# Performance work log

Measured on AMD Instinct MI355X. Metric: run time of the kernel, lower is better.

Reference implementation:

```python
import jax, jax.numpy as jnp
import numpy as np

EPS = 1e-5
NPOINT, K = 4096, 128
MLP = (64, 64, 128)
IN_CH = 3  # xyz only (Infea=0 -> use_feature=False)


def _conv_bn_relu(x, W, b, gamma, beta, mean, var):
    # 1x1 Conv2d == per-point channel GEMM: x [B,C,N,K], W [O,C]
    y = jnp.einsum('oc,bcnk->bonk', W, x) + b[None, :, None, None]
    inv = gamma / jnp.sqrt(var + EPS)
    y = y * inv[None, :, None, None] + (beta - mean * inv)[None, :, None, None]
    return jax.nn.relu(y)


def setup_inputs() -> dict:
    key = jax.random.key(0)
    ks = jax.random.split(key, 8)
    inp = {
        'grouped_pc': jax.random.normal(ks[0], (1, IN_CH, NPOINT, K), dtype=jnp.float32),
        'valid': (jax.random.uniform(ks[1], (1, 1, NPOINT, K)) > 0.3).astype(jnp.float32),
    }
    c_prev = IN_CH
    for i, c_out in enumerate(MLP, start=1):
        kw = jax.random.fold_in(ks[2], i)
        fan_in = c_prev  # kaiming_normal for 1x1 conv
        inp[f'W{i}'] = jax.random.normal(kw, (c_out, c_prev), dtype=jnp.float32) * np.sqrt(2.0 / fan_in)
        inp[f'b{i}'] = jnp.zeros((c_out,), dtype=jnp.float32)
        inp[f'gamma{i}'] = jnp.ones((c_out,), dtype=jnp.float32)
        inp[f'beta{i}'] = jnp.zeros((c_out,), dtype=jnp.float32)
        inp[f'mean{i}'] = jax.random.normal(jax.random.fold_in(ks[3], i), (c_out,), dtype=jnp.float32) * 0.1
        inp[f'var{i}'] = jax.random.uniform(jax.random.fold_in(ks[4], i), (c_out,), minval=0.5, maxval=1.5).astype(jnp.float32)
        c_prev = c_out
    return inp


def reference(grouped_pc, valid,
              W1, b1, gamma1, beta1, mean1, var1,
              W2, b2, gamma2, beta2, mean2, var2,
              W3, b3, gamma3, beta3, mean3, var3):
    x = _conv_bn_relu(grouped_pc, W1, b1, gamma1, beta1, mean1, var1)
    x = _conv_bn_relu(x, W2, b2, gamma2, beta2, mean2, var2)
    x = _conv_bn_relu(x, W3, b3, gamma3, beta3, mean3, var3)
    return x * valid  # validity mask broadcast over channels
```

## Files before the change

### kernel.cpp

```cpp
#include <hip/hip_runtime.h>
#include <math.h>

#define EPS 1e-5f
#define NPK (4096 * 128)

typedef __attribute__((ext_vector_type(8))) short bf16x8;
typedef __attribute__((ext_vector_type(4))) float f32x4;

__device__ __forceinline__ short f2bf(float f) {
    union { float f; unsigned u; } x; x.f = f;
    unsigned r = x.u + 0x7fffu + ((x.u >> 16) & 1u);
    return (short)(r >> 16);
}

#define WS_A1 0
#define WS_C1 192
#define WS_C2 256
#define WS_C3 320
#define WS_BF 448

__global__ void prep_kernel(
    const float* __restrict__ W1, const float* __restrict__ b1,
    const float* __restrict__ g1, const float* __restrict__ be1,
    const float* __restrict__ m1, const float* __restrict__ v1,
    const float* __restrict__ W2, const float* __restrict__ b2,
    const float* __restrict__ g2, const float* __restrict__ be2,
    const float* __restrict__ m2, const float* __restrict__ v2,
    const float* __restrict__ W3, const float* __restrict__ b3,
    const float* __restrict__ g3, const float* __restrict__ be3,
    const float* __restrict__ m3, const float* __restrict__ v3,
    float* __restrict__ ws)
{
    const int t = blockIdx.x * 256 + threadIdx.x;
    const int stride = gridDim.x * 256;
    if (t < 64) {
        float inv1 = g1[t] * rsqrtf(v1[t] + EPS);
        ws[WS_C1 + t] = b1[t] * inv1 + be1[t] - m1[t] * inv1;
        ws[WS_A1 + t * 3 + 0] = W1[t * 3 + 0] * inv1;
        ws[WS_A1 + t * 3 + 1] = W1[t * 3 + 1] * inv1;
        ws[WS_A1 + t * 3 + 2] = W1[t * 3 + 2] * inv1;
        float inv2 = g2[t] * rsqrtf(v2[t] + EPS);
        ws[WS_C2 + t] = b2[t] * inv2 + be2[t] - m2[t] * inv2;
    }
    if (t >= 128 && t < 256) {
        int o = t - 128;
        float inv3 = g3[o] * rsqrtf(v3[o] + EPS);
        ws[WS_C3 + o] = b3[o] * inv3 + be3[o] - m3[o] * inv3;
    }
    short* W2f = (short*)(ws + WS_BF);
    short* W3f = W2f + 64 * 64;
    for (int idx = t; idx < 64 * 64; idx += stride) {
        int j = idx & 7, lane = (idx >> 3) & 63, tile = idx >> 9;
        int nt = tile >> 1, ks = tile & 1;
        int o = nt * 16 + (lane & 15);
        int i = ks * 32 + (lane >> 4) * 8 + j;
        float inv = g2[o] * rsqrtf(v2[o] + EPS);
        W2f[idx] = f2bf(W2[o * 64 + i] * inv);
    }
    for (int idx = t; idx < 128 * 64; idx += stride) {
        int j = idx & 7, lane = (idx >> 3) & 63, tile = idx >> 9;
        int nt = tile >> 1, ks = tile & 1;
        int o = nt * 16 + (lane & 15);
        int i = ks * 32 + (lane >> 4) * 8 + j;
        float inv = g3[o] * rsqrtf(v3[o] + EPS);
        W3f[idx] = f2bf(W3[o * 64 + i] * inv);
    }
}

__global__ __launch_bounds__(256) void pointnet_mfma(
    const float* __restrict__ x, const float* __restrict__ valid,
    const float* __restrict__ ws, float* __restrict__ out)
{
    __shared__ short h1[128 * 72];
    __shared__ short h2[128 * 72];
    __shared__ float vld[128];

    const int t = threadIdx.x;
    const int pbase = blockIdx.x * 128;

    const float* __restrict__ A1 = ws + WS_A1;
    const float* __restrict__ C1 = ws + WS_C1;
    const float* __restrict__ C2 = ws + WS_C2;
    const float* __restrict__ C3 = ws + WS_C3;
    const short* __restrict__ W2f = (const short*)(ws + WS_BF);
    const short* __restrict__ W3f = W2f + 64 * 64;

    {
        const int pl = t & 127;
        const int half = t >> 7;
        const int pg = pbase + pl;
        const float x0 = x[pg];
        const float x1 = x[pg + NPK];
        const float x2 = x[pg + 2 * NPK];
        if (half == 0) vld[pl] = valid[pg];
        const int cb = half * 32;
#pragma unroll
        for (int g = 0; g < 4; ++g) {
            bf16x8 vb;
#pragma unroll
            for (int j = 0; j < 8; ++j) {
                const int ch = cb + g * 8 + j;
                float a = C1[ch];
                a = fmaf(A1[ch * 3 + 0], x0, a);
                a = fmaf(A1[ch * 3 + 1], x1, a);
                a = fmaf(A1[ch * 3 + 2], x2, a);
                vb[j] = f2bf(fmaxf(a, 0.0f));
            }
            *(bf16x8*)&h1[pl * 72 + cb + g * 8] = vb;
        }
    }
    __syncthreads();

    const int lane = t & 63;
    const int w = t >> 6;
    const int lanelo = lane & 15;
    const int quad = lane >> 4;

    {
        bf16x8 a[2][2];
#pragma unroll
        for (int mt = 0; mt < 2; ++mt)
#pragma unroll
            for (int ks = 0; ks < 2; ++ks)
                a[mt][ks] = *(const bf16x8*)&h1[(w * 32 + mt * 16 + lanelo) * 72 + ks * 32 + quad * 8];
#pragma unroll
        for (int nt = 0; nt < 4; ++nt) {
            bf16x8 b0 = *(const bf16x8*)&W2f[((nt * 2 + 0) * 64 + lane) * 8];
            bf16x8 b1 = *(const bf16x8*)&W2f[((nt * 2 + 1) * 64 + lane) * 8];
            const float bias = C2[nt * 16 + lanelo];
#pragma unroll
            for (int mt = 0; mt < 2; ++mt) {
                f32x4 acc = {0.f, 0.f, 0.f, 0.f};
                acc = __builtin_amdgcn_mfma_f32_16x16x32_bf16(a[mt][0], b0, acc, 0, 0, 0);
                acc = __builtin_amdgcn_mfma_f32_16x16x32_bf16(a[mt][1], b1, acc, 0, 0, 0);
#pragma unroll
                for (int r = 0; r < 4; ++r)
                    h2[(w * 32 + mt * 16 + quad * 4 + r) * 72 + nt * 16 + lanelo] =
                        f2bf(fmaxf(acc[r] + bias, 0.0f));
            }
        }
    }
    __syncthreads();

    {
        bf16x8 a[2][2];
#pragma unroll
        for (int mt = 0; mt < 2; ++mt)
#pragma unroll
            for (int ks = 0; ks < 2; ++ks)
                a[mt][ks] = *(const bf16x8*)&h2[(w * 32 + mt * 16 + lanelo) * 72 + ks * 32 + quad * 8];
        f32x4 v4[2];
        v4[0] = *(const f32x4*)&vld[w * 32 + quad * 4];
        v4[1] = *(const f32x4*)&vld[w * 32 + 16 + quad * 4];
#pragma unroll
        for (int nt = 0; nt < 8; ++nt) {
            bf16x8 b0 = *(const bf16x8*)&W3f[((nt * 2 + 0) * 64 + lane) * 8];
            bf16x8 b1 = *(const bf16x8*)&W3f[((nt * 2 + 1) * 64 + lane) * 8];
            const float bias = C3[nt * 16 + lanelo];
            const long chbase = (long)(nt * 16 + lanelo) * NPK;
#pragma unroll
            for (int mt = 0; mt < 2; ++mt) {
                f32x4 acc = {0.f, 0.f, 0.f, 0.f};
                acc = __builtin_amdgcn_mfma_f32_16x16x32_bf16(a[mt][0], b0, acc, 0, 0, 0);
                acc = __builtin_amdgcn_mfma_f32_16x16x32_bf16(a[mt][1], b1, acc, 0, 0, 0);
                f32x4 o;
#pragma unroll
                for (int r = 0; r < 4; ++r)
                    o[r] = fmaxf(acc[r] + bias, 0.0f) * v4[mt][r];
                *(f32x4*)&out[chbase + pbase + w * 32 + mt * 16 + quad * 4] = o;
            }
        }
    }
}

extern "C" void kernel_launch(void* const* d_in, const int* in_sizes, int n_in,
                              void* d_out, int out_size, void* d_ws, size_t ws_size,
                              hipStream_t stream) {
    const float* x     = (const float*)d_in[0];
    const float* valid = (const float*)d_in[1];

    const float* W1 = (const float*)d_in[2];
    const float* b1 = (const float*)d_in[3];
    const float* g1 = (const float*)d_in[4];
    const float* be1 = (const float*)d_in[5];
    const float* m1 = (const float*)d_in[6];
    const float* v1 = (const float*)d_in[7];

    const float* W2 = (const float*)d_in[8];
    const float* b2 = (const float*)d_in[9];
    const float* g2 = (const float*)d_in[10];
    const float* be2 = (const float*)d_in[11];
    const float* m2 = (const float*)d_in[12];
    const float* v2 = (const float*)d_in[13];

    const float* W3 = (const float*)d_in[14];
    const float* b3 = (const float*)d_in[15];
    const float* g3 = (const float*)d_in[16];
    const float* be3 = (const float*)d_in[17];
    const float* m3 = (const float*)d_in[18];
    const float* v3 = (const float*)d_in[19];

    float* ws  = (float*)d_ws;
    float* out = (float*)d_out;

    prep_kernel<<<16, 256, 0, stream>>>(W1, b1, g1, be1, m1, v1,
                                        W2, b2, g2, be2, m2, v2,
                                        W3, b3, g3, be3, m3, v3, ws);

    pointnet_mfma<<<NPK / 128, 256, 0, stream>>>(x, valid, ws, out);
}
```

Before: 339.0 us.

## Build layer-1 activations directly in MFMA registers and drop block barriers

The first conv layer is now computed by each lane straight into the bf16 A-operand fragments that the layer-2 MFMA consumes. This removes the h1 shared-memory buffer, its stores and loads, and the first __syncthreads. Because each wave only writes and reads its own rows of h2, the second barrier is also removed, and the validity mask is read straight from global memory instead of through LDS. The trade is more VGPR pressure from holding the fragments. It also depends on the compiler keeping LDS write-before-read ordering within a wave.

```diff
diff --git a/kernel.cpp b/kernel.cpp
--- a/kernel.cpp
+++ b/kernel.cpp
@@ -71,12 +71,14 @@
     const float* __restrict__ x, const float* __restrict__ valid,
     const float* __restrict__ ws, float* __restrict__ out)
 {
-    __shared__ short h1[128 * 72];
     __shared__ short h2[128 * 72];
-    __shared__ float vld[128];
 
     const int t = threadIdx.x;
     const int pbase = blockIdx.x * 128;
+    const int lane = t & 63;
+    const int w = t >> 6;
+    const int lanelo = lane & 15;
+    const int quad = lane >> 4;
 
     const float* __restrict__ A1 = ws + WS_A1;
     const float* __restrict__ C1 = ws + WS_C1;
@@ -85,73 +87,58 @@
     const short* __restrict__ W2f = (const short*)(ws + WS_BF);
     const short* __restrict__ W3f = W2f + 64 * 64;
 
+    bf16x8 a[2][2];
     {
-        const int pl = t & 127;
-        const int half = t >> 7;
-        const int pg = pbase + pl;
-        const float x0 = x[pg];
-        const float x1 = x[pg + NPK];
-        const float x2 = x[pg + 2 * NPK];
-        if (half == 0) vld[pl] = valid[pg];
-        const int cb = half * 32;
+        const int p0 = pbase + w * 32 + lanelo;
+        const float x00 = x[p0];
+        const float x01 = x[p0 + NPK];
+        const float x02 = x[p0 + 2 * NPK];
+        const float x10 = x[p0 + 16];
+        const float x11 = x[p0 + 16 + NPK];
+        const float x12 = x[p0 + 16 + 2 * NPK];
 #pragma unroll
-        for (int g = 0; g < 4; ++g) {
-            bf16x8 vb;
+        for (int ks = 0; ks < 2; ++ks)
 #pragma unroll
             for (int j = 0; j < 8; ++j) {
-                const int ch = cb + g * 8 + j;
-                float a = C1[ch];
-                a = fmaf(A1[ch * 3 + 0], x0, a);
-                a = fmaf(A1[ch * 3 + 1], x1, a);
-                a = fmaf(A1[ch * 3 + 2], x2, a);
-                vb[j] = f2bf(fmaxf(a, 0.0f));
+                const int ch = ks * 32 + quad * 8 + j;
+                const float wa = A1[ch * 3 + 0];
+                const float wb = A1[ch * 3 + 1];
+                const float wc = A1[ch * 3 + 2];
+                const float cc = C1[ch];
+                const float y0 = fmaf(wa, x00, fmaf(wb, x01, fmaf(wc, x02, cc)));
+                const float y1 = fmaf(wa, x10, fmaf(wb, x11, fmaf(wc, x12, cc)));
+                a[0][ks][j] = f2bf(fmaxf(y0, 0.0f));
+                a[1][ks][j] = f2bf(fmaxf(y1, 0.0f));
             }
-            *(bf16x8*)&h1[pl * 72 + cb + g * 8] = vb;
+    }
+
+#pragma unroll
+    for (int nt = 0; nt < 4; ++nt) {
+        bf16x8 b0 = *(const bf16x8*)&W2f[((nt * 2 + 0) * 64 + lane) * 8];
+        bf16x8 b1 = *(const bf16x8*)&W2f[((nt * 2 + 1) * 64 + lane) * 8];
+        const float bias = C2[nt * 16 + lanelo];
+#pragma unroll
+        for (int mt = 0; mt < 2; ++mt) {
+            f32x4 acc = {0.f, 0.f, 0.f, 0.f};
+            acc = __builtin_amdgcn_mfma_f32_16x16x32_bf16(a[mt][0], b0, acc, 0, 0, 0);
+            acc = __builtin_amdgcn_mfma_f32_16x16x32_bf16(a[mt][1], b1, acc, 0, 0, 0);
+#pragma unroll
+            for (int r = 0; r < 4; ++r)
+                h2[(w * 32 + mt * 16 + quad * 4 + r) * 72 + nt * 16 + lanelo] =
+                    f2bf(fmaxf(acc[r] + bias, 0.0f));
         }
     }
-    __syncthreads();
-
-    const int lane = t & 63;
-    const int w = t >> 6;
-    const int lanelo = lane & 15;
-    const int quad = lane >> 4;
 
     {
-        bf16x8 a[2][2];
+        bf16x8 a2[2][2];
 #pragma unroll
         for (int mt = 0; mt < 2; ++mt)
 #pragma unroll
             for (int ks = 0; ks < 2; ++ks)
-                a[mt][ks] = *(const bf16x8*)&h1[(w * 32 + mt * 16 + lanelo) * 72 + ks * 32 + quad * 8];
-#pragma unroll
-        for (int nt = 0; nt < 4; ++nt) {
-            bf16x8 b0 = *(const bf16x8*)&W2f[((nt * 2 + 0) * 64 + lane) * 8];
-            bf16x8 b1 = *(const bf16x8*)&W2f[((nt * 2 + 1) * 64 + lane) * 8];
-            const float bias = C2[nt * 16 + lanelo];
-#pragma unroll
-            for (int mt = 0; mt < 2; ++mt) {
-                f32x4 acc = {0.f, 0.f, 0.f, 0.f};
-                acc = __builtin_amdgcn_mfma_f32_16x16x32_bf16(a[mt][0], b0, acc, 0, 0, 0);
-                acc = __builtin_amdgcn_mfma_f32_16x16x32_bf16(a[mt][1], b1, acc, 0, 0, 0);
-#pragma unroll
-                for (int r = 0; r < 4; ++r)
-                    h2[(w * 32 + mt * 16 + quad * 4 + r) * 72 + nt * 16 + lanelo] =
-                        f2bf(fmaxf(acc[r] + bias, 0.0f));
-            }
-        }
-    }
-    __syncthreads();
-
-    {
-        bf16x8 a[2][2];
-#pragma unroll
-        for (int mt = 0; mt < 2; ++mt)
-#pragma unroll
-            for (int ks = 0; ks < 2; ++ks)
-                a[mt][ks] = *(const bf16x8*)&h2[(w * 32 + mt * 16 + lanelo) * 72 + ks * 32 + quad * 8];
+                a2[mt][ks] = *(const bf16x8*)&h2[(w * 32 + mt * 16 + lanelo) * 72 + ks * 32 + quad * 8];
         f32x4 v4[2];
-        v4[0] = *(const f32x4*)&vld[w * 32 + quad * 4];
-        v4[1] = *(const f32x4*)&vld[w * 32 + 16 + quad * 4];
+        v4[0] = *(const f32x4*)&valid[pbase + w * 32 + quad * 4];
+        v4[1] = *(const f32x4*)&valid[pbase + w * 32 + 16 + quad * 4];
 #pragma unroll
         for (int nt = 0; nt < 8; ++nt) {
             bf16x8 b0 = *(const bf16x8*)&W3f[((nt * 2 + 0) * 64 + lane) * 8];
@@ -161,8 +148,8 @@
 #pragma unroll
             for (int mt = 0; mt < 2; ++mt) {
                 f32x4 acc = {0.f, 0.f, 0.f, 0.f};
-                acc = __builtin_amdgcn_mfma_f32_16x16x32_bf16(a[mt][0], b0, acc, 0, 0, 0);
-                acc = __builtin_amdgcn_mfma_f32_16x16x32_bf16(a[mt][1], b1, acc, 0, 0, 0);
+                acc = __builtin_amdgcn_mfma_f32_16x16x32_bf16(a2[mt][0], b0, acc, 0, 0, 0);
+                acc = __builtin_amdgcn_mfma_f32_16x16x32_bf16(a2[mt][1], b1, acc, 0, 0, 0);
                 f32x4 o;
 #pragma unroll
                 for (int r = 0; r < 4; ++r)
```

Measured after the change: 342.5 us. No clear change (+1.0%).
